# Optimization experiments

Hardware: AMD Instinct MI355X
Metric: run time of the kernel (lower is better)

Reference implementation:

```python
import jax, jax.numpy as jnp
import numpy as np
import math

B, T, C, H, ORDER = 2, 192, 512, 8, 3
HS = C // H  # head_size = 64


def setup_inputs() -> dict:
    key = jax.random.key(0)
    ks = jax.random.split(key, 12)
    init = lambda k, shape: (0.02 * jax.random.normal(k, shape, jnp.float32))
    return {
        "x0": jax.random.normal(ks[0], (B, T, C), jnp.float32),
        "x1": jax.random.normal(ks[1], (B, T, C), jnp.float32),
        "x2": jax.random.normal(ks[2], (B, T, C), jnp.float32),
        # per-head, per-modality Linear(C -> HS): weights (H, ORDER, HS, C), biases (H, ORDER, HS)
        "qw": init(ks[3], (H, ORDER, HS, C)), "qb": init(ks[4], (H, ORDER, HS)),
        "kw": init(ks[5], (H, ORDER, HS, C)), "kb": init(ks[6], (H, ORDER, HS)),
        "vw": init(ks[7], (H, ORDER, HS, C)), "vb": init(ks[8], (H, ORDER, HS)),
        # output projection Linear(C -> C)
        "cw": init(ks[9], (C, C)), "cb": init(ks[10], (C,)),
    }


def _proj(x, w, b):
    # x: (B,T,C), w: (H,HS,C), b: (H,HS) -> (B,H,T,HS)
    return jnp.einsum("btc,hdc->bhtd", x, w) + b[None, :, None, :]


def reference(x0, x1, x2, qw, qb, kw, kb, vw, vb, cw, cb):
    # order=3: query factor from x0, key factors from x1,x2, value factors from x1,x2
    Q0 = _proj(x0, qw[:, 0], qb[:, 0])  # (B,H,T0,HS)
    K1 = _proj(x1, kw[:, 1], kb[:, 1])  # (B,H,T1,HS)
    K2 = _proj(x2, kw[:, 2], kb[:, 2])  # (B,H,T2,HS)
    V1 = _proj(x1, vw[:, 1], vb[:, 1])  # (B,H,T1,HS)
    V2 = _proj(x2, vw[:, 2], vb[:, 2])  # (B,H,T2,HS)

    scale = 1.0 / math.sqrt(HS)
    # order-3 attention tensor: A[b,h,i,j,k] = sum_d Q0*K1*K2
    A = jnp.einsum("bhid,bhjd,bhkd->bhijk", Q0, K1, K2) * scale
    b, h, t0, t1, t2 = A.shape
    # softmax over the flattened (j,k) key dims, as in the torch code
    A = jax.nn.softmax(A.reshape(b, h, t0, t1 * t2), axis=-1).reshape(b, h, t0, t1, t2)
    # contract with outer-product-merged V: merged_V[b,j,k,d] = V1[b,j,d]*V2[b,k,d]
    Y = jnp.einsum("bhijk,bhjd,bhkd->bhid", A, V1, V2)  # (B,H,T0,HS)
    out = jnp.transpose(Y, (0, 2, 1, 3)).reshape(b, t0, h * HS)  # stack heads -> (B,T0,C)
    return out @ cw.T + cb
```

## Files before the change

kernel.cpp:

```cpp
#include <hip/hip_runtime.h>

typedef float f4v __attribute__((ext_vector_type(4)));
typedef _Float16 h2v __attribute__((ext_vector_type(2)));
typedef _Float16 h4v __attribute__((ext_vector_type(4)));
typedef _Float16 h8v __attribute__((ext_vector_type(8)));
typedef __fp16 g4 __attribute__((ext_vector_type(4)));
typedef __fp16 g8 __attribute__((ext_vector_type(8)));
typedef unsigned short u16;
typedef unsigned int u32;

#define SPLIT 8
#define ESC 0.18033688011112042f

__device__ __forceinline__ h2v pkh(float lo, float hi) {
  return __builtin_bit_cast(h2v, __builtin_amdgcn_cvt_pkrtz(lo, hi));
}
__device__ __forceinline__ f4v mfma_k32(h8v a, h8v b, f4v c) {
  return __builtin_amdgcn_mfma_f32_16x16x32_f16(
      __builtin_bit_cast(g8, a), __builtin_bit_cast(g8, b), c, 0, 0, 0);
}
__device__ __forceinline__ f4v mfma_k16(h4v a, h4v b, f4v c) {
  return __builtin_amdgcn_mfma_f32_16x16x16f16(
      __builtin_bit_cast(g4, a), __builtin_bit_cast(g4, b), c, 0, 0, 0);
}

__global__ __launch_bounds__(256) void proj_kernel(
    const float* __restrict__ x0, const float* __restrict__ x1,
    const float* __restrict__ x2,
    const float* __restrict__ qw, const float* __restrict__ qb,
    const float* __restrict__ kw, const float* __restrict__ kb,
    const float* __restrict__ vw, const float* __restrict__ vb,
    u16* __restrict__ Q0h, u16* __restrict__ K1h, float* __restrict__ V1f,
    u16* __restrict__ K2b, u16* __restrict__ V2b) {
  __shared__ float xs[32][36];
  __shared__ float wsh[32][68];

  int bx = blockIdx.x;
  int slot = bx / 96;
  int rem = bx - slot * 96;
  int bh = rem / 6;
  int tt = rem - bh * 6;
  int b = bh >> 3, h = bh & 7;
  int t0 = tt * 32;

  const float* x; const float* w; const float* bias; int o;
  float* outf = nullptr; u16* outb = nullptr;
  switch (slot) {
    case 0: x = x0; w = qw; bias = qb; o = 0; outb = Q0h; break;
    case 1: x = x1; w = kw; bias = kb; o = 1; outb = K1h; break;
    case 2: x = x2; w = kw; bias = kb; o = 2; outb = K2b; break;
    case 3: x = x1; w = vw; bias = vb; o = 1; outf = V1f; break;
    default: x = x2; w = vw; bias = vb; o = 2; outb = V2b; break;
  }
  x += b * 192 * 512;
  w += (h * 3 + o) * 64 * 512;
  bias += (h * 3 + o) * 64;

  int tid = threadIdx.x;
  int m2 = tid >> 4, nq = tid & 15;
  int mA = tid >> 3, clA = (tid & 7) * 4;
  int nB0 = tid >> 3, nB1 = (256 + tid) >> 3;
  float acc[2][4] = {};

  float4 pX, pW0, pW1;
  pX = *(const float4*)(x + (t0 + mA) * 512 + clA);
  pW0 = *(const float4*)(w + nB0 * 512 + clA);
  pW1 = *(const float4*)(w + nB1 * 512 + clA);

  for (int kc = 0; kc < 16; ++kc) {
    xs[clA][mA] = pX.x; xs[clA + 1][mA] = pX.y;
    xs[clA + 2][mA] = pX.z; xs[clA + 3][mA] = pX.w;
    wsh[clA][nB0] = pW0.x; wsh[clA + 1][nB0] = pW0.y;
    wsh[clA + 2][nB0] = pW0.z; wsh[clA + 3][nB0] = pW0.w;
    wsh[clA][nB1] = pW1.x; wsh[clA + 1][nB1] = pW1.y;
    wsh[clA + 2][nB1] = pW1.z; wsh[clA + 3][nB1] = pW1.w;
    __syncthreads();
    if (kc < 15) {
      int cb0 = (kc + 1) * 32;
      pX = *(const float4*)(x + (t0 + mA) * 512 + cb0 + clA);
      pW0 = *(const float4*)(w + nB0 * 512 + cb0 + clA);
      pW1 = *(const float4*)(w + nB1 * 512 + cb0 + clA);
    }
#pragma unroll
    for (int c = 0; c < 32; ++c) {
      float2 av = *(const float2*)&xs[c][m2 * 2];
      float4 bv = *(const float4*)&wsh[c][nq * 4];
      acc[0][0] += av.x * bv.x; acc[0][1] += av.x * bv.y;
      acc[0][2] += av.x * bv.z; acc[0][3] += av.x * bv.w;
      acc[1][0] += av.y * bv.x; acc[1][1] += av.y * bv.y;
      acc[1][2] += av.y * bv.z; acc[1][3] += av.y * bv.w;
    }
    __syncthreads();
  }

  float4 bias4 = *(const float4*)(bias + nq * 4);
#pragma unroll
  for (int i = 0; i < 2; ++i) {
    int t = t0 + m2 * 2 + i;
    long base = ((long)(bh * 192 + t)) * 64 + nq * 4;
    float o0 = acc[i][0] + bias4.x;
    float o1 = acc[i][1] + bias4.y;
    float o2 = acc[i][2] + bias4.z;
    float o3 = acc[i][3] + bias4.w;
    if (slot == 0) {
      o0 *= ESC; o1 *= ESC; o2 *= ESC; o3 *= ESC;
    }
    if (outf) {
      float4 st = {o0, o1, o2, o3};
      *(float4*)(outf + base) = st;
    } else {
      h2v a = pkh(o0, o1), c2 = pkh(o2, o3);
      uint2 st = {__builtin_bit_cast(u32, a), __builtin_bit_cast(u32, c2)};
      *(uint2*)(outb + base) = st;
    }
  }
}

__global__ __launch_bounds__(256, 4) void attn_kernel(
    const u16* __restrict__ Q0h, const u16* __restrict__ K1h,
    const float* __restrict__ V1f, const u16* __restrict__ K2b,
    const u16* __restrict__ V2b, float* __restrict__ Op,
    float* __restrict__ lp) {
  __shared__ __align__(16) char smem[25856];
  int bx = blockIdx.x;
  int sp = bx / 192;
  int rem = bx - sp * 192;
  int bh = rem / 12;
  int itile = rem - bh * 12;
  int i0 = itile * 16;
  int js = sp * 24;
  int tid = threadIdx.x;
  int wave = tid >> 6;
  int lane = tid & 63;
  int l15 = lane & 15;
  int quad = lane >> 4;

  u16* K1s = (u16*)smem;
  float* V1s = (float*)(smem + 3072);

  u32 kreg0, kreg1, kreg2;
  float2 vreg0, vreg1, vreg2;
  {
    const u32* ksrc = (const u32*)(K1h + (bh * 192 + js) * 64);
    kreg0 = ksrc[tid]; kreg1 = ksrc[256 + tid]; kreg2 = ksrc[512 + tid];
    const float2* vsrc2 = (const float2*)(V1f + (bh * 192 + js) * 64);
    vreg0 = vsrc2[tid]; vreg1 = vsrc2[256 + tid]; vreg2 = vsrc2[512 + tid];
  }

  u16* V2T = (u16*)smem;
  {
    const u32* vsrc = (const u32*)V2b + bh * 6144;
#pragma unroll
    for (int r = 0; r < 24; ++r) {
      int idx = r * 256 + tid;
      int k = idx >> 5, d2 = idx & 31;
      u32 v = vsrc[idx];
      V2T[(d2 * 2) * 202 + k] = (u16)v;
      V2T[(d2 * 2 + 1) * 202 + k] = (u16)(v >> 16);
    }
  }
  h8v k2f[3][2];
#pragma unroll
  for (int nt = 0; nt < 3; ++nt)
#pragma unroll
    for (int ks = 0; ks < 2; ++ks)
      k2f[nt][ks] = *(const h8v*)(K2b +
          (bh * 192 + wave * 48 + nt * 16 + l15) * 64 + ks * 32 + quad * 8);
  const u16* qq = Q0h + (bh * 192 + i0 + l15) * 64 + quad * 8;
  h8v qh0 = *(const h8v*)qq;
  h8v qh1 = *(const h8v*)(qq + 32);
  __syncthreads();
  h8v v2g0[4]; h4v v2g1[4];
#pragma unroll
  for (int dt = 0; dt < 4; ++dt) {
    const char* p = smem + (dt * 16 + l15) * 404 + wave * 96 + quad * 8;
    union { h8v v; u32 w[4]; } u0;
    u0.w[0] = *(const u32*)p;        u0.w[1] = *(const u32*)(p + 4);
    u0.w[2] = *(const u32*)(p + 32); u0.w[3] = *(const u32*)(p + 36);
    v2g0[dt] = u0.v;
    union { h4v v; u32 w[2]; } u1;
    u1.w[0] = *(const u32*)(p + 64); u1.w[1] = *(const u32*)(p + 68);
    v2g1[dt] = u1.v;
  }
  __syncthreads();
  ((u32*)K1s)[tid] = kreg0;
  ((u32*)K1s)[256 + tid] = kreg1;
  ((u32*)K1s)[512 + tid] = kreg2;
  ((float2*)V1s)[tid] = vreg0;
  ((float2*)V1s)[256 + tid] = vreg1;
  ((float2*)V1s)[512 + tid] = vreg2;
  __syncthreads();

  f4v Oacc[4] = {};
  float lsum = 0.f;
  const f4v z = {0.f, 0.f, 0.f, 0.f};

#pragma unroll 1
  for (int j = 0; j < 24; ++j) {
    h8v c0 = *(const h8v*)(K1s + j * 64 + quad * 8);
    h8v c1 = *(const h8v*)(K1s + j * 64 + 32 + quad * 8);
    h8v B0 = qh0 * c0, B1 = qh1 * c1;
    f4v s0 = mfma_k32(k2f[0][0], B0, z);
    f4v s1 = mfma_k32(k2f[1][0], B0, z);
    f4v s2 = mfma_k32(k2f[2][0], B0, z);
    s0 = mfma_k32(k2f[0][1], B1, s0);
    s1 = mfma_k32(k2f[1][1], B1, s1);
    s2 = mfma_k32(k2f[2][1], B1, s2);
    float p[12];
#pragma unroll
    for (int r = 0; r < 4; ++r) {
      p[r] = __builtin_amdgcn_exp2f(s0[r]);
      p[4 + r] = __builtin_amdgcn_exp2f(s1[r]);
      p[8 + r] = __builtin_amdgcn_exp2f(s2[r]);
    }
    lsum += (((p[0] + p[1]) + (p[2] + p[3])) + ((p[4] + p[5]) + (p[6] + p[7]))) +
            ((p[8] + p[9]) + (p[10] + p[11]));
    union { h8v v; h2v h[4]; } pa0;
    pa0.h[0] = pkh(p[0], p[1]);  pa0.h[1] = pkh(p[2], p[3]);
    pa0.h[2] = pkh(p[4], p[5]);  pa0.h[3] = pkh(p[6], p[7]);
    union { h4v v; h2v h[2]; } pa1;
    pa1.h[0] = pkh(p[8], p[9]);  pa1.h[1] = pkh(p[10], p[11]);
    float v1r0 = V1s[j * 64 + l15];
    float v1r1 = V1s[j * 64 + 16 + l15];
    float v1r2 = V1s[j * 64 + 32 + l15];
    float v1r3 = V1s[j * 64 + 48 + l15];
#pragma unroll
    for (int dt = 0; dt < 4; ++dt) {
      f4v w = mfma_k32(pa0.v, v2g0[dt], z);
      w = mfma_k16(pa1.v, v2g1[dt], w);
      float v1x = dt == 0 ? v1r0 : dt == 1 ? v1r1 : dt == 2 ? v1r2 : v1r3;
      Oacc[dt][0] = fmaf(v1x, w[0], Oacc[dt][0]);
      Oacc[dt][1] = fmaf(v1x, w[1], Oacc[dt][1]);
      Oacc[dt][2] = fmaf(v1x, w[2], Oacc[dt][2]);
      Oacc[dt][3] = fmaf(v1x, w[3], Oacc[dt][3]);
    }
  }

  __syncthreads();
  float* ored = (float*)smem;
  float* lred = (float*)(smem + 16384);
  float* ow = ored + wave * 1024;
#pragma unroll
  for (int dt = 0; dt < 4; ++dt)
#pragma unroll
    for (int r = 0; r < 4; ++r)
      ow[(quad * 4 + r) * 64 + dt * 16 + l15] = Oacc[dt][r];
  lsum += __shfl_xor(lsum, 16);
  lsum += __shfl_xor(lsum, 32);
  if (quad == 0) lred[wave * 16 + l15] = lsum;
  __syncthreads();
  f4v s = *(const f4v*)(ored + tid * 4);
  s += *(const f4v*)(ored + 1024 + tid * 4);
  s += *(const f4v*)(ored + 2048 + tid * 4);
  s += *(const f4v*)(ored + 3072 + tid * 4);
  *(f4v*)(Op + ((long)(sp * 16 + bh) * 192 + i0) * 64 + tid * 4) = s;
  if (tid < 16)
    lp[(sp * 16 + bh) * 192 + i0 + tid] =
        lred[tid] + lred[16 + tid] + lred[32 + tid] + lred[48 + tid];
}

__global__ __launch_bounds__(256) void outproj_kernel(
    const float* __restrict__ Op, const float* __restrict__ lp,
    const float* __restrict__ cw, const float* __restrict__ cb,
    float* __restrict__ out) {
  __shared__ float xs[32][20];
  __shared__ float wsh[32][68];
  __shared__ float linv[8][16];
  int bx = blockIdx.x;
  int mt = bx >> 3, nt = bx & 7;
  int m0 = mt * 16;
  int b = m0 / 192;
  int t0 = m0 - b * 192;
  int n0 = nt * 64;
  int tid = threadIdx.x;

  if (tid < 128) {
    int h = tid >> 4, ml = tid & 15;
    float s = 0.f;
#pragma unroll
    for (int sp = 0; sp < SPLIT; ++sp)
      s += lp[(sp * 16 + b * 8 + h) * 192 + t0 + ml];
    linv[h][ml] = 1.0f / s;
  }

  int mA = tid >> 3, clA = (tid & 7) * 4;
  int nB0 = tid >> 3, nB1 = (256 + tid) >> 3;
  int m = tid >> 4, nq = tid & 15;
  float acc[4] = {};

  float4 pA[SPLIT];
  float4 pW0, pW1;
  {
    if (tid < 128) {
#pragma unroll
      for (int sp = 0; sp < SPLIT; ++sp)
        pA[sp] = *(const float4*)(
            Op + (long)((sp * 16 + b * 8) * 192 + t0 + mA) * 64 + clA);
    }
    pW0 = *(const float4*)(cw + (long)(n0 + nB0) * 512 + clA);
    pW1 = *(const float4*)(cw + (long)(n0 + nB1) * 512 + clA);
  }
  __syncthreads();

  for (int kc = 0; kc < 16; ++kc) {
    int h = kc >> 1;
    if (tid < 128) {
      float4 s = pA[0];
#pragma unroll
      for (int sp = 1; sp < SPLIT; ++sp) {
        s.x += pA[sp].x; s.y += pA[sp].y; s.z += pA[sp].z; s.w += pA[sp].w;
      }
      float li = linv[h][mA];
      xs[clA][mA] = s.x * li; xs[clA + 1][mA] = s.y * li;
      xs[clA + 2][mA] = s.z * li; xs[clA + 3][mA] = s.w * li;
    }
    wsh[clA][nB0] = pW0.x; wsh[clA + 1][nB0] = pW0.y;
    wsh[clA + 2][nB0] = pW0.z; wsh[clA + 3][nB0] = pW0.w;
    wsh[clA][nB1] = pW1.x; wsh[clA + 1][nB1] = pW1.y;
    wsh[clA + 2][nB1] = pW1.z; wsh[clA + 3][nB1] = pW1.w;
    __syncthreads();
    if (kc < 15) {
      int h2 = (kc + 1) >> 1, d2 = ((kc + 1) & 1) * 32;
      if (tid < 128) {
#pragma unroll
        for (int sp = 0; sp < SPLIT; ++sp)
          pA[sp] = *(const float4*)(
              Op + (long)((sp * 16 + b * 8 + h2) * 192 + t0 + mA) * 64 + d2 +
              clA);
      }
      pW0 = *(const float4*)(cw + (long)(n0 + nB0) * 512 + h2 * 64 + d2 + clA);
      pW1 = *(const float4*)(cw + (long)(n0 + nB1) * 512 + h2 * 64 + d2 + clA);
    }
#pragma unroll
    for (int c = 0; c < 32; ++c) {
      float a = xs[c][m];
      float4 bv = *(const float4*)&wsh[c][nq * 4];
      acc[0] += a * bv.x; acc[1] += a * bv.y;
      acc[2] += a * bv.z; acc[3] += a * bv.w;
    }
    __syncthreads();
  }

  float4 bias = *(const float4*)(cb + n0 + nq * 4);
  float4 st;
  st.x = acc[0] + bias.x;
  st.y = acc[1] + bias.y;
  st.z = acc[2] + bias.z;
  st.w = acc[3] + bias.w;
  *(float4*)(out + (long)(b * 192 + t0 + m) * 512 + n0 + nq * 4) = st;
}

extern "C" void kernel_launch(void* const* d_in, const int* in_sizes, int n_in,
                              void* d_out, int out_size, void* d_ws, size_t ws_size,
                              hipStream_t stream) {
  const float* x0 = (const float*)d_in[0];
  const float* x1 = (const float*)d_in[1];
  const float* x2 = (const float*)d_in[2];
  const float* qw = (const float*)d_in[3];
  const float* qb = (const float*)d_in[4];
  const float* kw = (const float*)d_in[5];
  const float* kb = (const float*)d_in[6];
  const float* vb2 = (const float*)d_in[8];
  const float* vw = (const float*)d_in[7];
  const float* cw = (const float*)d_in[9];
  const float* cb = (const float*)d_in[10];
  float* out = (float*)d_out;

  char* ws = (char*)d_ws;
  u16* Q0h = (u16*)(ws + 0);
  u16* K1h = (u16*)(ws + 393216);
  float* V1f = (float*)(ws + 786432);
  u16* K2b = (u16*)(ws + 1572864);
  u16* V2b = (u16*)(ws + 1966080);
  float* Op = (float*)(ws + 2359296);
  float* lp = (float*)(ws + 2359296 + (size_t)SPLIT * 786432);

  proj_kernel<<<480, 256, 0, stream>>>(x0, x1, x2, qw, qb, kw, kb, vw, vb2,
                                       Q0h, K1h, V1f, K2b, V2b);
  attn_kernel<<<SPLIT * 192, 256, 0, stream>>>(Q0h, K1h, V1f, K2b, V2b,
                                               Op, lp);
  outproj_kernel<<<192, 256, 0, stream>>>(Op, lp, cw, cb, out);
}
```

Measured before the change: 155.2 us.

## Convert inputs to fp16 in a prep pass and run projections on MFMA

Adds a prep kernel that converts x0/x1/x2 and all q/k/v weights to fp16 in workspace. The projection kernel is rewritten so each wave computes a 16x16 output tile with 16x16x32 f16 MFMA instructions read straight from global memory, with no shared memory. This replaces the scalar fp32 LDS-tiled GEMM. It adds an extra kernel launch, a full read and write of every weight each call, and fp16 rounding of the inputs.

Measured after the change: 146.5 us. 5.6% less time.

```diff
diff --git a/kernel.cpp b/kernel.cpp
--- a/kernel.cpp
+++ b/kernel.cpp
@@ -24,95 +24,87 @@
       __builtin_bit_cast(g4, a), __builtin_bit_cast(g4, b), c, 0, 0, 0);
 }
 
-__global__ __launch_bounds__(256) void proj_kernel(
+__global__ __launch_bounds__(256) void prep_kernel(
     const float* __restrict__ x0, const float* __restrict__ x1,
     const float* __restrict__ x2,
-    const float* __restrict__ qw, const float* __restrict__ qb,
-    const float* __restrict__ kw, const float* __restrict__ kb,
-    const float* __restrict__ vw, const float* __restrict__ vb,
+    const float* __restrict__ qw, const float* __restrict__ kw,
+    const float* __restrict__ vw,
+    u16* __restrict__ xh, u16* __restrict__ wh) {
+  int i = blockIdx.x * 256 + threadIdx.x;
+  const int total = 1474560;
+  for (; i < total; i += gridDim.x * 256) {
+    const float* s; int off; u16* d;
+    if (i < 294912) {
+      int seg = i / 98304;
+      s = seg == 0 ? x0 : seg == 1 ? x1 : x2;
+      off = i - seg * 98304;
+      d = xh + seg * 196608;
+    } else {
+      int j = i - 294912;
+      int seg = j / 393216;
+      s = seg == 0 ? qw : seg == 1 ? kw : vw;
+      off = j - seg * 393216;
+      d = wh + seg * 786432;
+    }
+    float2 v = *(const float2*)(s + (long)off * 2);
+    *(u32*)(d + (long)off * 2) = __builtin_bit_cast(u32, pkh(v.x, v.y));
+  }
+}
+
+__global__ __launch_bounds__(256) void proj_kernel(
+    const u16* __restrict__ xh, const u16* __restrict__ wh,
+    const float* __restrict__ qb, const float* __restrict__ kb,
+    const float* __restrict__ vb,
     u16* __restrict__ Q0h, u16* __restrict__ K1h, float* __restrict__ V1f,
     u16* __restrict__ K2b, u16* __restrict__ V2b) {
-  __shared__ float xs[32][36];
-  __shared__ float wsh[32][68];
-
-  int bx = blockIdx.x;
-  int slot = bx / 96;
-  int rem = bx - slot * 96;
-  int bh = rem / 6;
-  int tt = rem - bh * 6;
+  int g = blockIdx.x * 4 + (threadIdx.x >> 6);
+  int lane = threadIdx.x & 63;
+  int l15 = lane & 15, quad = lane >> 4;
+  int slot = g / 768;
+  int rem = g - slot * 768;
+  int bh = rem / 48;
+  int r2 = rem - bh * 48;
+  int tt = r2 >> 2, dt = r2 & 3;
   int b = bh >> 3, h = bh & 7;
-  int t0 = tt * 32;
-
-  const float* x; const float* w; const float* bias; int o;
+
+  int xsel, o, wsel;
+  const float* bias;
   float* outf = nullptr; u16* outb = nullptr;
   switch (slot) {
-    case 0: x = x0; w = qw; bias = qb; o = 0; outb = Q0h; break;
-    case 1: x = x1; w = kw; bias = kb; o = 1; outb = K1h; break;
-    case 2: x = x2; w = kw; bias = kb; o = 2; outb = K2b; break;
-    case 3: x = x1; w = vw; bias = vb; o = 1; outf = V1f; break;
-    default: x = x2; w = vw; bias = vb; o = 2; outb = V2b; break;
-  }
-  x += b * 192 * 512;
-  w += (h * 3 + o) * 64 * 512;
-  bias += (h * 3 + o) * 64;
-
-  int tid = threadIdx.x;
-  int m2 = tid >> 4, nq = tid & 15;
-  int mA = tid >> 3, clA = (tid & 7) * 4;
-  int nB0 = tid >> 3, nB1 = (256 + tid) >> 3;
-  float acc[2][4] = {};
-
-  float4 pX, pW0, pW1;
-  pX = *(const float4*)(x + (t0 + mA) * 512 + clA);
-  pW0 = *(const float4*)(w + nB0 * 512 + clA);
-  pW1 = *(const float4*)(w + nB1 * 512 + clA);
-
+    case 0: xsel = 0; o = 0; wsel = 0; bias = qb; outb = Q0h; break;
+    case 1: xsel = 1; o = 1; wsel = 1; bias = kb; outb = K1h; break;
+    case 2: xsel = 2; o = 2; wsel = 1; bias = kb; outb = K2b; break;
+    case 3: xsel = 1; o = 1; wsel = 2; bias = vb; outf = V1f; break;
+    default: xsel = 2; o = 2; wsel = 2; bias = vb; outb = V2b; break;
+  }
+  const u16* xp = xh + (long)xsel * 196608 +
+                  ((long)(b * 192 + tt * 16 + l15)) * 512;
+  const u16* wp = wh + (long)wsel * 786432 +
+                  ((long)((h * 3 + o) * 64 + dt * 16 + l15)) * 512;
+  bias += (h * 3 + o) * 64 + dt * 16;
+
+  f4v acc = {0.f, 0.f, 0.f, 0.f};
+#pragma unroll 4
   for (int kc = 0; kc < 16; ++kc) {
-    xs[clA][mA] = pX.x; xs[clA + 1][mA] = pX.y;
-    xs[clA + 2][mA] = pX.z; xs[clA + 3][mA] = pX.w;
-    wsh[clA][nB0] = pW0.x; wsh[clA + 1][nB0] = pW0.y;
-    wsh[clA + 2][nB0] = pW0.z; wsh[clA + 3][nB0] = pW0.w;
-    wsh[clA][nB1] = pW1.x; wsh[clA + 1][nB1] = pW1.y;
-    wsh[clA + 2][nB1] = pW1.z; wsh[clA + 3][nB1] = pW1.w;
-    __syncthreads();
-    if (kc < 15) {
-      int cb0 = (kc + 1) * 32;
-      pX = *(const float4*)(x + (t0 + mA) * 512 + cb0 + clA);
-      pW0 = *(const float4*)(w + nB0 * 512 + cb0 + clA);
-      pW1 = *(const float4*)(w + nB1 * 512 + cb0 + clA);
-    }
-#pragma unroll
-    for (int c = 0; c < 32; ++c) {
-      float2 av = *(const float2*)&xs[c][m2 * 2];
-      float4 bv = *(const float4*)&wsh[c][nq * 4];
-      acc[0][0] += av.x * bv.x; acc[0][1] += av.x * bv.y;
-      acc[0][2] += av.x * bv.z; acc[0][3] += av.x * bv.w;
-      acc[1][0] += av.y * bv.x; acc[1][1] += av.y * bv.y;
-      acc[1][2] += av.y * bv.z; acc[1][3] += av.y * bv.w;
-    }
-    __syncthreads();
-  }
-
-  float4 bias4 = *(const float4*)(bias + nq * 4);
-#pragma unroll
-  for (int i = 0; i < 2; ++i) {
-    int t = t0 + m2 * 2 + i;
-    long base = ((long)(bh * 192 + t)) * 64 + nq * 4;
-    float o0 = acc[i][0] + bias4.x;
-    float o1 = acc[i][1] + bias4.y;
-    float o2 = acc[i][2] + bias4.z;
-    float o3 = acc[i][3] + bias4.w;
-    if (slot == 0) {
-      o0 *= ESC; o1 *= ESC; o2 *= ESC; o3 *= ESC;
-    }
-    if (outf) {
-      float4 st = {o0, o1, o2, o3};
-      *(float4*)(outf + base) = st;
-    } else {
-      h2v a = pkh(o0, o1), c2 = pkh(o2, o3);
-      uint2 st = {__builtin_bit_cast(u32, a), __builtin_bit_cast(u32, c2)};
-      *(uint2*)(outb + base) = st;
-    }
+    h8v a = *(const h8v*)(wp + kc * 32 + quad * 8);
+    h8v bf = *(const h8v*)(xp + kc * 32 + quad * 8);
+    acc = mfma_k32(a, bf, acc);
+  }
+
+  float4 b4 = *(const float4*)(bias + quad * 4);
+  int t = tt * 16 + l15;
+  int d = dt * 16 + quad * 4;
+  long base = ((long)(bh * 192 + t)) * 64 + d;
+  float o0 = acc[0] + b4.x, o1 = acc[1] + b4.y;
+  float o2 = acc[2] + b4.z, o3 = acc[3] + b4.w;
+  if (slot == 0) { o0 *= ESC; o1 *= ESC; o2 *= ESC; o3 *= ESC; }
+  if (outf) {
+    float4 st = {o0, o1, o2, o3};
+    *(float4*)(outf + base) = st;
+  } else {
+    uint2 st = {__builtin_bit_cast(u32, pkh(o0, o1)),
+                __builtin_bit_cast(u32, pkh(o2, o3))};
+    *(uint2*)(outb + base) = st;
   }
 }
 
@@ -360,8 +352,8 @@
   const float* qb = (const float*)d_in[4];
   const float* kw = (const float*)d_in[5];
   const float* kb = (const float*)d_in[6];
-  const float* vb2 = (const float*)d_in[8];
   const float* vw = (const float*)d_in[7];
+  const float* vb = (const float*)d_in[8];
   const float* cw = (const float*)d_in[9];
   const float* cb = (const float*)d_in[10];
   float* out = (float*)d_out;
@@ -374,8 +366,11 @@
   u16* V2b = (u16*)(ws + 1966080);
   float* Op = (float*)(ws + 2359296);
   float* lp = (float*)(ws + 2359296 + (size_t)SPLIT * 786432);
-
-  proj_kernel<<<480, 256, 0, stream>>>(x0, x1, x2, qw, qb, kw, kb, vw, vb2,
+  u16* xh = (u16*)(ws + 9437184);
+  u16* wh = (u16*)(ws + 9437184 + 1179648);
+
+  prep_kernel<<<1440, 256, 0, stream>>>(x0, x1, x2, qw, kw, vw, xh, wh);
+  proj_kernel<<<960, 256, 0, stream>>>(xh, wh, qb, kb, vb,
                                        Q0h, K1h, V1f, K2b, V2b);
   attn_kernel<<<SPLIT * 192, 256, 0, stream>>>(Q0h, K1h, V1f, K2b, V2b,
                                                Op, lp);
```
